# Kernel optimization log

Hardware: AMD Instinct MI355X
Metric: run time of the kernel (lower is better)

## Reference

```python
import jax, jax.numpy as jnp
import numpy as np

KH = KW = 3
PAD = 1
OFFG = 8  # offset groups: 144 offset channels / (2*9)


def conv2d(x, w, b, pad=PAD):
    out = jax.lax.conv_general_dilated(
        x, w, window_strides=(1, 1), padding=[(pad, pad), (pad, pad)],
        dimension_numbers=('NCHW', 'OIHW', 'NCHW'))
    return out + b[None, :, None, None]


def deform_conv2d(x, offset, w, b):
    # x: [B,C,H,W], offset: [B, 2*K*OFFG, H, W] (per group: (y,x) per kernel tap)
    B, C, H, W = x.shape
    K = KH * KW
    Cg = C // OFFG
    off = offset.reshape(B, OFFG, K, 2, H, W)
    ky, kx = jnp.meshgrid(jnp.arange(KH), jnp.arange(KW), indexing='ij')
    ky = ky.reshape(K).astype(x.dtype)
    kx = kx.reshape(K).astype(x.dtype)
    ys = (jnp.arange(H) - PAD).astype(x.dtype)  # stride 1, dilation 1
    xs = (jnp.arange(W) - PAD).astype(x.dtype)
    # sampling positions [B, OFFG, K, H, W]
    py = ys[None, None, None, :, None] + ky[None, None, :, None, None] + off[:, :, :, 0]
    px = xs[None, None, None, None, :] + kx[None, None, :, None, None] + off[:, :, :, 1]
    y0 = jnp.floor(py)
    x0 = jnp.floor(px)
    xg = x.reshape(B, OFFG, Cg, H * W)
    cols = jnp.zeros((B, OFFG, Cg, K, H, W), x.dtype)
    for dy in (0, 1):
        for dx in (0, 1):
            yi = y0 + dy
            xi = x0 + dx
            wgt = (1.0 - jnp.abs(py - yi)) * (1.0 - jnp.abs(px - xi))
            valid = (yi >= 0) & (yi < H) & (xi >= 0) & (xi < W)
            yc = jnp.clip(yi, 0, H - 1).astype(jnp.int32)
            xc = jnp.clip(xi, 0, W - 1).astype(jnp.int32)
            idx = (yc * W + xc).reshape(B, OFFG, 1, K * H * W)
            g = jnp.take_along_axis(xg, idx, axis=3).reshape(B, OFFG, Cg, K, H, W)
            cols = cols + g * (wgt * valid.astype(x.dtype))[:, :, None]
    cols = cols.reshape(B, C, K, H, W)
    out = jnp.einsum('bckhw,ock->bohw', cols, w.reshape(w.shape[0], C, K))
    return out + b[None, :, None, None]


def setup_inputs() -> dict:
    key = jax.random.key(0)
    ks = jax.random.split(key, 6)
    B, C, H, W = 16, 144, 64, 64
    feat_arm = jax.random.normal(ks[0], (B, C, H, W), jnp.float32)
    feat_up = jax.random.normal(ks[1], (B, C, H, W), jnp.float32)
    # offset conv: in=288 (cat), out=144 = 2*9*OFFG; small init so offsets are sane
    off_w = jax.random.normal(ks[2], (144, 288, 3, 3), jnp.float32) * 0.01
    off_b = jnp.zeros((144,), jnp.float32)
    dcn_w = jax.random.normal(ks[3], (256, 144, 3, 3), jnp.float32) * (1.0 / np.sqrt(144 * 9))
    dcn_b = jnp.zeros((256,), jnp.float32)
    return {'feat_arm': feat_arm, 'feat_up': feat_up, 'off_w': off_w,
            'off_b': off_b, 'dcn_w': dcn_w, 'dcn_b': dcn_b}


def reference(feat_arm, feat_up, off_w, off_b, dcn_w, dcn_b):
    x = jnp.concatenate([feat_arm, feat_up], axis=1)  # [B, 288, H, W]
    offset = conv2d(x, off_w, off_b)                  # [B, 144, H, W]
    y = deform_conv2d(feat_up, offset, dcn_w, dcn_b)  # [B, 256, H, W]
    return jax.nn.silu(y)
```

## Files before the change

### kernel.cpp

```cpp
#include <hip/hip_runtime.h>
#include <math.h>

constexpr int BN = 16;
constexpr int C_IN = 144, C_CAT = 288, C_OFF = 144, C_OUT = 256;
constexpr int OFFG = 8, CG = 18;

constexpr int OFF_ELEMS = BN * C_OFF * 64 * 64;
constexpr int WOFF_PACK = 9 * 9 * 9 * 512;
constexpr int WDCN_PACK = 8 * 6 * 16 * 512;

typedef __attribute__((ext_vector_type(8))) short bf16x8;
typedef __attribute__((ext_vector_type(4))) float f32x4;

__device__ __forceinline__ unsigned short f2bf(float f) {
  unsigned u = __builtin_bit_cast(unsigned, f);
  return (unsigned short)((u + 0x7FFFu + ((u >> 16) & 1u)) >> 16);
}

__device__ __forceinline__ unsigned packh2(float a, float b) {
  unsigned short ha = __builtin_bit_cast(unsigned short, (_Float16)a);
  unsigned short hb = __builtin_bit_cast(unsigned short, (_Float16)b);
  return (unsigned)ha | ((unsigned)hb << 16);
}
__device__ __forceinline__ float h2f_lo(unsigned u) {
  return (float)__builtin_bit_cast(_Float16, (unsigned short)(u & 0xFFFFu));
}
__device__ __forceinline__ float h2f_hi(unsigned u) {
  return (float)__builtin_bit_cast(_Float16, (unsigned short)(u >> 16));
}

__device__ __forceinline__ void gload_lds16(const void* g, void* l) {
  __builtin_amdgcn_global_load_lds(
      (const __attribute__((address_space(1))) unsigned*)g,
      (__attribute__((address_space(3))) unsigned*)l, 16, 0, 0);
}

__global__ __launch_bounds__(256) void pack_w(
    const float* __restrict__ off_w, const float* __restrict__ dcn_w,
    unsigned short* __restrict__ wo, unsigned short* __restrict__ wd) {
  int idx = blockIdx.x * 256 + threadIdx.x;
  if (idx < WOFF_PACK) {
    int i = idx & 7, lane = (idx >> 3) & 63, t = idx >> 9;
    int mt = t % 9; t /= 9;
    int tap = t % 9, cb = t / 9;
    int co = mt * 16 + (lane & 15);
    int ci = cb * 32 + ((lane >> 4) << 3) + i;
    wo[idx] = f2bf(off_w[(co * C_CAT + ci) * 9 + tap]);
  }
  if (idx < WDCN_PACK) {
    int i = idx & 7, lane = (idx >> 3) & 63, t = idx >> 9;
    int mt = t & 15; t >>= 4;
    int ks = t % 6, g = t / 6;
    int co = mt * 16 + (lane & 15);
    int r = ks * 32 + ((lane >> 4) << 3) + i;
    float v = 0.f;
    if (r < 162) {
      int ci = r / 9, tap = r - ci * 9;
      v = dcn_w[(co * C_IN + g * CG + ci) * 9 + tap];
    }
    wd[idx] = f2bf(v);
  }
}

__global__ __launch_bounds__(256) void offs_conv_mfma(
    const float* __restrict__ fa, const float* __restrict__ fu,
    const unsigned short* __restrict__ wt, const float* __restrict__ bias,
    float* __restrict__ out) {
  const int b = blockIdx.x >> 5;
  const int y0 = (blockIdx.x & 31) << 1;
  const int tid = threadIdx.x;
  const int wave = tid >> 6, lane = tid & 63;
  const int kg = lane >> 4, ln = lane & 15;

  __shared__ __align__(16) unsigned short xs[4 * 66 * 32];

  f32x4 acc[9][2];
#pragma unroll
  for (int m = 0; m < 9; ++m)
#pragma unroll
    for (int n = 0; n < 2; ++n) acc[m][n] = {0.f, 0.f, 0.f, 0.f};

  for (int cb = 0; cb < 9; ++cb) {
    __syncthreads();
    for (int idx = tid; idx < 2112; idx += 256) {
      int q = idx / 264;
      int rem = idx - q * 264;
      int row = rem / 66;
      int cc = rem - row * 66;
      int y = y0 - 1 + row, x = cc - 1;
      ushort4 wv = make_ushort4(0, 0, 0, 0);
      if (y >= 0 && y < 64 && x >= 0 && x < 64) {
        int cib = cb * 32 + (q << 2);
        const float* p = (cib < C_IN)
                             ? fa + (((size_t)(b * C_IN + cib)) << 12)
                             : fu + (((size_t)(b * C_IN + cib - C_IN)) << 12);
        int o = (y << 6) + x;
        wv.x = f2bf(p[o]);
        wv.y = f2bf(p[o + 4096]);
        wv.z = f2bf(p[o + 8192]);
        wv.w = f2bf(p[o + 12288]);
      }
      int e = ((row * 66 + cc) << 5) + (((q >> 1) ^ (cc & 3)) << 3) + ((q & 1) << 2);
      *(ushort4*)&xs[e] = wv;
    }
    __syncthreads();

    for (int tap = 0; tap < 9; ++tap) {
      const int ky = tap / 3, kx = tap - ky * 3;
      bf16x8 a[9];
      const unsigned short* wp = wt + (((size_t)(cb * 9 + tap) * 9) << 9) + (lane << 3);
#pragma unroll
      for (int m = 0; m < 9; ++m) a[m] = *(const bf16x8*)(wp + (m << 9));
#pragma unroll
      for (int n = 0; n < 2; ++n) {
        int px = ((wave << 1) + n) * 16 + ln;
        int row = (px >> 6) + ky, cc = (px & 63) + kx;
        int e = ((row * 66 + cc) << 5) + ((kg ^ (cc & 3)) << 3);
        bf16x8 bv = *(const bf16x8*)&xs[e];
#pragma unroll
        for (int m = 0; m < 9; ++m)
          acc[m][n] = __builtin_amdgcn_mfma_f32_16x16x32_bf16(a[m], bv, acc[m][n], 0, 0, 0);
      }
    }
  }

#pragma unroll
  for (int n = 0; n < 2; ++n) {
    int px = ((wave << 1) + n) * 16 + ln;
    int y = y0 + (px >> 6), x = px & 63;
#pragma unroll
    for (int m = 0; m < 9; ++m) {
      int cob = m * 16 + (kg << 2);
#pragma unroll
      for (int r = 0; r < 4; ++r)
        out[(((size_t)(b * C_OFF + cob + r)) << 12) + (y << 6) + x] =
            acc[m][n][r] + bias[cob + r];
    }
  }
}

__global__ __launch_bounds__(512, 4) void dcn_mfma(
    const float* __restrict__ fu, const float* __restrict__ off,
    const unsigned short* __restrict__ wt, const float* __restrict__ bias,
    float* __restrict__ out) {
  const int b = blockIdx.x >> 6, h = blockIdx.x & 63;
  const int tid = threadIdx.x;
  const int wave = tid >> 6, lane = tid & 63;
  const int kg = lane >> 4, ln = lane & 15;
  const int wm = wave >> 2, wn = wave & 3;
  const int px = (wn << 4) + ln;

  __shared__ __align__(16) unsigned short colsT[64 * 200];
  __shared__ __align__(16) unsigned short wl[2][8192];

  f32x4 acc[8];
#pragma unroll
  for (int m = 0; m < 8; ++m) acc[m] = {0.f, 0.f, 0.f, 0.f};

  for (int i = tid; i < 64 * 19; i += 512) {
    int p = i / 19, d = i - p * 19;
    *(unsigned*)&colsT[p * 200 + 162 + 2 * d] = 0u;
  }

  {
    const unsigned short* src = wt + (wave * 2) * 512 + lane * 8;
#pragma unroll
    for (int j = 0; j < 2; ++j)
      gload_lds16(src + j * 512, &wl[0][(wave * 2 + j) * 512]);
  }

  auto make_geo = [&](int gg_, int tap, int p) -> uint4 {
    int ky = tap / 3, kx = tap - ky * 3;
    int ch = (gg_ * 9 + tap) * 2;
    float oy = off[(((size_t)(b * C_OFF + ch)) << 12) + (h << 6) + p];
    float ox = off[(((size_t)(b * C_OFF + ch + 1)) << 12) + (h << 6) + p];
    float py = (float)(h - 1 + ky) + oy;
    float pxs = (float)(p - 1 + kx) + ox;
    float y0f = floorf(py), x0f = floorf(pxs);
    int y0 = (int)y0f, x0 = (int)x0f;
    float fy = py - y0f, fx = pxs - x0f;
    float vy0 = (y0 >= 0 && y0 < 64) ? 1.f : 0.f;
    float vy1 = (y0 + 1 >= 0 && y0 + 1 < 64) ? 1.f : 0.f;
    float vx0 = (x0 >= 0 && x0 < 64) ? 1.f : 0.f;
    float vx1 = (x0 + 1 >= 0 && x0 + 1 < 64) ? 1.f : 0.f;
    float a0 = (1.f - fx) * vx0;
    float a1 = fx * vx1;
    float wlo = (x0 == -1) ? a1 : (x0 == 63 ? 0.f : a0);
    float whi = (x0 == 63) ? a0 : (x0 == -1 ? 0.f : a1);
    int xL = min(max(x0, 0), 62);
    int yc0 = min(max(y0, 0), 63), yc1 = min(max(y0 + 1, 0), 63);
    float cy0 = (1.f - fy) * vy0, cy1 = fy * vy1;
    uint4 r;
    r.x = (unsigned)((yc0 << 6) + xL) | ((unsigned)((yc1 << 6) + xL) << 16);
    r.y = 0u;
    r.z = packh2(cy0 * wlo, cy0 * whi);
    r.w = packh2(cy1 * wlo, cy1 * whi);
    return r;
  };

  int t = 0;
  for (int g = 0; g < OFFG; ++g) {
    __syncthreads();

    uint4 gg = make_geo(g, wave, lane);
    uint4 g8 = make_geo(g, 8, lane);

    const float* gbase = fu + (((size_t)(b * C_IN + g * CG)) << 12);
    {
      const int iL0 = gg.x & 0xFFFFu, iL1 = gg.x >> 16;
      const float wl0 = h2f_lo(gg.z), wh0 = h2f_hi(gg.z);
      const float wl1 = h2f_lo(gg.w), wh1 = h2f_hi(gg.w);
      for (int cb = 0; cb < 18; cb += 6) {
        float2 v0[6], v1[6];
#pragma unroll
        for (int u = 0; u < 6; ++u) {
          const float* pl = gbase + ((size_t)(cb + u) << 12);
          __builtin_memcpy(&v0[u], pl + iL0, 8);
          __builtin_memcpy(&v1[u], pl + iL1, 8);
        }
#pragma unroll
        for (int u = 0; u < 6; ++u) {
          float s = wl0 * v0[u].x + wh0 * v0[u].y + wl1 * v1[u].x + wh1 * v1[u].y;
          colsT[lane * 200 + (cb + u) * 9 + wave] = f2bf(s);
        }
      }
      const int j0 = g8.x & 0xFFFFu, j1 = g8.x >> 16;
      const float ul0 = h2f_lo(g8.z), uh0 = h2f_hi(g8.z);
      const float ul1 = h2f_lo(g8.w), uh1 = h2f_hi(g8.w);
      const int n8 = (wave < 2) ? 3 : 2;
      float2 w0[3], w1[3];
#pragma unroll
      for (int u = 0; u < 3; ++u) {
        if (u < n8) {
          const float* pl = gbase + ((size_t)(wave + 8 * u) << 12);
          __builtin_memcpy(&w0[u], pl + j0, 8);
          __builtin_memcpy(&w1[u], pl + j1, 8);
        }
      }
#pragma unroll
      for (int u = 0; u < 3; ++u) {
        if (u < n8) {
          float s = ul0 * w0[u].x + uh0 * w0[u].y + ul1 * w1[u].x + uh1 * w1[u].y;
          colsT[lane * 200 + (wave + 8 * u) * 9 + 8] = f2bf(s);
        }
      }
    }
    __syncthreads();

    for (int ks = 0; ks < 6; ++ks, ++t) {
      bf16x8 bv = *(const bf16x8*)&colsT[px * 200 + ks * 32 + (kg << 3)];

      __syncthreads();

      if (t < 47) {
        const unsigned short* src =
            wt + (size_t)(t + 1) * 8192 + (wave * 2) * 512 + lane * 8;
        unsigned short* dst = wl[(t + 1) & 1];
#pragma unroll
        for (int j = 0; j < 2; ++j)
          gload_lds16(src + j * 512, dst + (wave * 2 + j) * 512);
      }

      const unsigned short* wbuf = wl[t & 1] + (wm * 8) * 512 + lane * 8;
#pragma unroll
      for (int j = 0; j < 8; ++j) {
        bf16x8 av = *(const bf16x8*)(wbuf + j * 512);
        acc[j] = __builtin_amdgcn_mfma_f32_16x16x32_bf16(av, bv, acc[j], 0, 0, 0);
      }
    }
  }

#pragma unroll
  for (int j = 0; j < 8; ++j) {
    int cob = (wm * 8 + j) * 16 + (kg << 2);
#pragma unroll
    for (int r = 0; r < 4; ++r) {
      float y = acc[j][r] + bias[cob + r];
      out[(((size_t)(b * C_OUT + cob + r)) << 12) + (h << 6) + px] =
          y / (1.f + expf(-y));
    }
  }
}

extern "C" void kernel_launch(void* const* d_in, const int* in_sizes, int n_in,
                              void* d_out, int out_size, void* d_ws, size_t ws_size,
                              hipStream_t stream) {
  const float* feat_arm = (const float*)d_in[0];
  const float* feat_up  = (const float*)d_in[1];
  const float* off_w    = (const float*)d_in[2];
  const float* off_b    = (const float*)d_in[3];
  const float* dcn_w    = (const float*)d_in[4];
  const float* dcn_b    = (const float*)d_in[5];
  float* out = (float*)d_out;

  float* ws = (float*)d_ws;
  float* offbuf = ws;
  unsigned short* wo = (unsigned short*)(ws + OFF_ELEMS);
  unsigned short* wd = wo + WOFF_PACK;

  pack_w<<<(WDCN_PACK + 255) / 256, 256, 0, stream>>>(off_w, dcn_w, wo, wd);
  offs_conv_mfma<<<BN * 32, 256, 0, stream>>>(feat_arm, feat_up, wo, off_b, offbuf);
  dcn_mfma<<<BN * 64, 512, 0, stream>>>(feat_up, offbuf, wd, dcn_b, out);
}
```

Measured before the change: 298.1 us.

## Gather deformable samples from bf16 feature copy and store offsets as packed fp16

Adds a pre-pass that converts feat_up to bf16 so the bilinear gather in the deformable conv loads 4-byte pairs instead of 8-byte pairs. The offset conv now writes (y,x) offsets packed as fp16 pairs into one 32-bit word, halving offset traffic and the number of offset loads. The colsT row stride changes from 200 to 202, with B-fragment reads split into 32-bit loads, presumably to reduce LDS bank conflicts. Costs are an extra conversion kernel pass over feat_up, slightly reduced precision in offsets, and unaligned 4-byte reads.

```diff
diff --git a/kernel.cpp b/kernel.cpp
--- a/kernel.cpp
+++ b/kernel.cpp
@@ -5,12 +5,15 @@
 constexpr int C_IN = 144, C_CAT = 288, C_OFF = 144, C_OUT = 256;
 constexpr int OFFG = 8, CG = 18;
 
-constexpr int OFF_ELEMS = BN * C_OFF * 64 * 64;
+constexpr int FUB_ELEMS  = C_IN * BN * 4096;
+constexpr int OFFP_ELEMS = BN * 72 * 4096;
 constexpr int WOFF_PACK = 9 * 9 * 9 * 512;
 constexpr int WDCN_PACK = 8 * 6 * 16 * 512;
 
 typedef __attribute__((ext_vector_type(8))) short bf16x8;
 typedef __attribute__((ext_vector_type(4))) float f32x4;
+typedef __attribute__((ext_vector_type(2))) _Float16 f16x2;
+typedef __attribute__((ext_vector_type(4))) unsigned u32x4;
 
 __device__ __forceinline__ unsigned short f2bf(float f) {
   unsigned u = __builtin_bit_cast(unsigned, f);
@@ -28,11 +31,26 @@
 __device__ __forceinline__ float h2f_hi(unsigned u) {
   return (float)__builtin_bit_cast(_Float16, (unsigned short)(u >> 16));
 }
+__device__ __forceinline__ float bf_lo(unsigned u) {
+  return __builtin_bit_cast(float, u << 16);
+}
+__device__ __forceinline__ float bf_hi(unsigned u) {
+  return __builtin_bit_cast(float, u & 0xFFFF0000u);
+}
 
 __device__ __forceinline__ void gload_lds16(const void* g, void* l) {
   __builtin_amdgcn_global_load_lds(
       (const __attribute__((address_space(1))) unsigned*)g,
       (__attribute__((address_space(3))) unsigned*)l, 16, 0, 0);
+}
+
+__global__ __launch_bounds__(256) void tobf16_fu(
+    const float* __restrict__ fu, unsigned short* __restrict__ fuB) {
+  int i = (blockIdx.x * 256 + threadIdx.x) * 4;
+  float4 v = *(const float4*)(fu + i);
+  ushort4 o;
+  o.x = f2bf(v.x); o.y = f2bf(v.y); o.z = f2bf(v.z); o.w = f2bf(v.w);
+  *(ushort4*)(fuB + i) = o;
 }
 
 __global__ __launch_bounds__(256) void pack_w(
@@ -65,7 +83,7 @@
 __global__ __launch_bounds__(256) void offs_conv_mfma(
     const float* __restrict__ fa, const float* __restrict__ fu,
     const unsigned short* __restrict__ wt, const float* __restrict__ bias,
-    float* __restrict__ out) {
+    unsigned* __restrict__ offp) {
   const int b = blockIdx.x >> 5;
   const int y0 = (blockIdx.x & 31) << 1;
   const int tid = threadIdx.x;
@@ -132,15 +150,17 @@
     for (int m = 0; m < 9; ++m) {
       int cob = m * 16 + (kg << 2);
 #pragma unroll
-      for (int r = 0; r < 4; ++r)
-        out[(((size_t)(b * C_OFF + cob + r)) << 12) + (y << 6) + x] =
-            acc[m][n][r] + bias[cob + r];
+      for (int rr = 0; rr < 4; rr += 2) {
+        unsigned v = packh2(acc[m][n][rr] + bias[cob + rr],
+                            acc[m][n][rr + 1] + bias[cob + rr + 1]);
+        offp[(((size_t)(b * 72 + ((cob + rr) >> 1))) << 12) + (y << 6) + x] = v;
+      }
     }
   }
 }
 
 __global__ __launch_bounds__(512, 4) void dcn_mfma(
-    const float* __restrict__ fu, const float* __restrict__ off,
+    const unsigned short* __restrict__ fuB, const unsigned* __restrict__ offp,
     const unsigned short* __restrict__ wt, const float* __restrict__ bias,
     float* __restrict__ out) {
   const int b = blockIdx.x >> 6, h = blockIdx.x & 63;
@@ -150,16 +170,16 @@
   const int wm = wave >> 2, wn = wave & 3;
   const int px = (wn << 4) + ln;
 
-  __shared__ __align__(16) unsigned short colsT[64 * 200];
+  __shared__ __align__(16) unsigned short colsT[64 * 202];
   __shared__ __align__(16) unsigned short wl[2][8192];
 
   f32x4 acc[8];
 #pragma unroll
   for (int m = 0; m < 8; ++m) acc[m] = {0.f, 0.f, 0.f, 0.f};
 
-  for (int i = tid; i < 64 * 19; i += 512) {
-    int p = i / 19, d = i - p * 19;
-    *(unsigned*)&colsT[p * 200 + 162 + 2 * d] = 0u;
+  for (int i = tid; i < 64 * 15; i += 512) {
+    int p = i / 15, d = i - p * 15;
+    *(unsigned*)&colsT[p * 202 + 162 + 2 * d] = 0u;
   }
 
   {
@@ -171,9 +191,8 @@
 
   auto make_geo = [&](int gg_, int tap, int p) -> uint4 {
     int ky = tap / 3, kx = tap - ky * 3;
-    int ch = (gg_ * 9 + tap) * 2;
-    float oy = off[(((size_t)(b * C_OFF + ch)) << 12) + (h << 6) + p];
-    float ox = off[(((size_t)(b * C_OFF + ch + 1)) << 12) + (h << 6) + p];
+    unsigned op = offp[(((size_t)(b * 72 + gg_ * 9 + tap)) << 12) + (h << 6) + p];
+    float oy = h2f_lo(op), ox = h2f_hi(op);
     float py = (float)(h - 1 + ky) + oy;
     float pxs = (float)(p - 1 + kx) + ox;
     float y0f = floorf(py), x0f = floorf(pxs);
@@ -205,50 +224,58 @@
     uint4 gg = make_geo(g, wave, lane);
     uint4 g8 = make_geo(g, 8, lane);
 
-    const float* gbase = fu + (((size_t)(b * C_IN + g * CG)) << 12);
+    const unsigned short* gbase = fuB + (((size_t)(b * C_IN + g * CG)) << 12);
     {
       const int iL0 = gg.x & 0xFFFFu, iL1 = gg.x >> 16;
       const float wl0 = h2f_lo(gg.z), wh0 = h2f_hi(gg.z);
       const float wl1 = h2f_lo(gg.w), wh1 = h2f_hi(gg.w);
       for (int cb = 0; cb < 18; cb += 6) {
-        float2 v0[6], v1[6];
+        unsigned d0[6], d1[6];
 #pragma unroll
         for (int u = 0; u < 6; ++u) {
-          const float* pl = gbase + ((size_t)(cb + u) << 12);
-          __builtin_memcpy(&v0[u], pl + iL0, 8);
-          __builtin_memcpy(&v1[u], pl + iL1, 8);
+          const unsigned short* pl = gbase + ((size_t)(cb + u) << 12);
+          __builtin_memcpy(&d0[u], pl + iL0, 4);
+          __builtin_memcpy(&d1[u], pl + iL1, 4);
         }
 #pragma unroll
         for (int u = 0; u < 6; ++u) {
-          float s = wl0 * v0[u].x + wh0 * v0[u].y + wl1 * v1[u].x + wh1 * v1[u].y;
-          colsT[lane * 200 + (cb + u) * 9 + wave] = f2bf(s);
+          float s = wl0 * bf_lo(d0[u]) + wh0 * bf_hi(d0[u]) +
+                    wl1 * bf_lo(d1[u]) + wh1 * bf_hi(d1[u]);
+          colsT[lane * 202 + (cb + u) * 9 + wave] = f2bf(s);
         }
       }
       const int j0 = g8.x & 0xFFFFu, j1 = g8.x >> 16;
       const float ul0 = h2f_lo(g8.z), uh0 = h2f_hi(g8.z);
       const float ul1 = h2f_lo(g8.w), uh1 = h2f_hi(g8.w);
       const int n8 = (wave < 2) ? 3 : 2;
-      float2 w0[3], w1[3];
+      unsigned e0[3], e1[3];
 #pragma unroll
       for (int u = 0; u < 3; ++u) {
         if (u < n8) {
-          const float* pl = gbase + ((size_t)(wave + 8 * u) << 12);
-          __builtin_memcpy(&w0[u], pl + j0, 8);
-          __builtin_memcpy(&w1[u], pl + j1, 8);
+          const unsigned short* pl = gbase + ((size_t)(wave + 8 * u) << 12);
+          __builtin_memcpy(&e0[u], pl + j0, 4);
+          __builtin_memcpy(&e1[u], pl + j1, 4);
         }
       }
 #pragma unroll
       for (int u = 0; u < 3; ++u) {
         if (u < n8) {
-          float s = ul0 * w0[u].x + uh0 * w0[u].y + ul1 * w1[u].x + uh1 * w1[u].y;
-          colsT[lane * 200 + (wave + 8 * u) * 9 + 8] = f2bf(s);
+          float s = ul0 * bf_lo(e0[u]) + uh0 * bf_hi(e0[u]) +
+                    ul1 * bf_lo(e1[u]) + uh1 * bf_hi(e1[u]);
+          colsT[lane * 202 + (wave + 8 * u) * 9 + 8] = f2bf(s);
         }
       }
     }
     __syncthreads();
 
     for (int ks = 0; ks < 6; ++ks, ++t) {
-      bf16x8 bv = *(const bf16x8*)&colsT[px * 200 + ks * 32 + (kg << 3)];
+      int cbase = px * 202 + ks * 32 + (kg << 3);
+      u32x4 bu;
+      bu[0] = *(const unsigned*)&colsT[cbase];
+      bu[1] = *(const unsigned*)&colsT[cbase + 2];
+      bu[2] = *(const unsigned*)&colsT[cbase + 4];
+      bu[3] = *(const unsigned*)&colsT[cbase + 6];
+      bf16x8 bv = __builtin_bit_cast(bf16x8, bu);
 
       __syncthreads();
 
@@ -293,12 +320,13 @@
   const float* dcn_b    = (const float*)d_in[5];
   float* out = (float*)d_out;
 
-  float* ws = (float*)d_ws;
-  float* offbuf = ws;
-  unsigned short* wo = (unsigned short*)(ws + OFF_ELEMS);
+  unsigned short* fuB = (unsigned short*)d_ws;
+  unsigned* offp = (unsigned*)(fuB + FUB_ELEMS);
+  unsigned short* wo = (unsigned short*)(offp + OFFP_ELEMS);
   unsigned short* wd = wo + WOFF_PACK;
 
+  tobf16_fu<<<FUB_ELEMS / 1024, 256, 0, stream>>>(feat_up, fuB);
   pack_w<<<(WDCN_PACK + 255) / 256, 256, 0, stream>>>(off_w, dcn_w, wo, wd);
-  offs_conv_mfma<<<BN * 32, 256, 0, stream>>>(feat_arm, feat_up, wo, off_b, offbuf);
-  dcn_mfma<<<BN * 64, 512, 0, stream>>>(feat_up, offbuf, wd, dcn_b, out);
-}
+  offs_conv_mfma<<<BN * 32, 256, 0, stream>>>(feat_arm, feat_up, wo, off_b, offp);
+  dcn_mfma<<<BN * 64, 512, 0, stream>>>(fuB, offp, wd, dcn_b, out);
+}
```

Result: faster. 269.3 us (-9.6%).
